# Performance work log

Hardware: AMD Instinct MI355X
Metric: run time of the kernel (lower is better)

The kernel has to match this reference:

```python
import jax, jax.numpy as jnp
import numpy as np

IMG = 224
PS = 2
C_IN = 3
EMBED = 768
BATCH = 256
SLICES = IMG // 2            # 112
L = 2 * (SLICES // PS)       # 112 levels
K = IMG * PS                 # 448 gathered (a,b) pairs per level
D_IN = K * C_IN              # 1344


def _build_levels(n=IMG, slices=SLICES, ps=PS):
    """Replicates LUnraveling index construction (natural order; set() in the
    original only permutes within a level, which is equivalent up to a fixed
    permutation of weight columns for random init)."""
    a_list, b_list = [], []
    ar = np.arange(n)
    for i in range(slices // ps):
        cols = range(i * ps, (i + 1) * ps)
        # 'up' level: pairs (j, col) for j in range(n), concatenated over ps cols
        a_list.append(np.concatenate([ar for _ in cols]))
        b_list.append(np.concatenate([np.full(n, c) for c in cols]))
        # 'right' level: pairs (n - slices + col, j) for j in range(n)
        a_list.append(np.concatenate([np.full(n, n - slices + c) for c in cols]))
        b_list.append(np.concatenate([ar for _ in cols]))
    return (np.stack(a_list).astype(np.int32), np.stack(b_list).astype(np.int32))


def setup_inputs() -> dict:
    key = jax.random.key(0)
    k1, k2, k3 = jax.random.split(key, 3)
    x = jax.random.normal(k1, (BATCH, C_IN, IMG, IMG), dtype=jnp.float32)
    W = jax.random.normal(k2, (EMBED, D_IN), dtype=jnp.float32) * (1.0 / np.sqrt(D_IN))
    b = jax.random.normal(k3, (EMBED,), dtype=jnp.float32) * 0.01
    a_np, b_np = _build_levels()
    return {"x": x, "W": W, "b": b,
            "a_idx": jnp.asarray(a_np), "b_idx": jnp.asarray(b_np)}


def reference(x, W, b, a_idx, b_idx):
    B = x.shape[0]
    # gather: x[:, :, a, b] with (L,K) index arrays -> (B, C, L, K)
    g = x[:, :, a_idx, b_idx]
    # per-level flatten(1) in torch flattens (C, K) C-major -> (B, L, C*K)
    g = jnp.transpose(g, (0, 2, 1, 3)).reshape(B, L, C_IN * K)
    # shared linear projection per level token
    tokens = jnp.einsum('bld,ed->ble', g, W) + b
    return tokens  # (B, L, EMBED); norm is Identity (norm_layer=None)
```

## Files before the change

kernel.cpp:

```cpp
#include <hip/hip_runtime.h>
#include <stdint.h>


#define IMG   224
#define NLEV  112
#define CIN   3
#define DIN   1344
#define EMB   768
#define BATCH 256
#define MTOT  28672
#define NT    21

#define BM    128
#define BN    128
#define BK    64
#define LDP   72

#define AS1 __attribute__((address_space(1)))
#define AS3 __attribute__((address_space(3)))

typedef __attribute__((ext_vector_type(8))) short   short8;
typedef __attribute__((ext_vector_type(4))) float   floatx4;

__device__ __forceinline__ unsigned short f2bf(float f) {
    unsigned u = __float_as_uint(f);
    unsigned r = (u + 0x7fffu + ((u >> 16) & 1u)) >> 16;
    return (unsigned short)r;
}
__device__ __forceinline__ float bf2f(unsigned short s) {
    return __uint_as_float(((unsigned)s) << 16);
}
__device__ __forceinline__ unsigned pack2(float a, float b) {
    return (unsigned)f2bf(a) | ((unsigned)f2bf(b) << 16);
}

__global__ void detect_dtype(const unsigned short* __restrict__ W, int* flag) {
    __shared__ int s;
    if (threadIdx.x == 0) s = 0;
    __syncthreads();
    int bad = 0;
    for (int k = threadIdx.x; k < 4096; k += 256) {
        unsigned v = (unsigned)W[2 * k] & 0x7FFFu;
        if (v >= 0x4000u) bad = 1;
    }
    if (bad) atomicOr(&s, 1);
    __syncthreads();
    if (threadIdx.x == 0) *flag = s;
}

__global__ __launch_bounds__(256)
void pack_w(const void* __restrict__ Wv, const void* __restrict__ Bv,
            unsigned short* __restrict__ Wb, float* __restrict__ Bf,
            const int* __restrict__ flag)
{
    const bool F32 = (*flag != 0);
    const int idx = blockIdx.x * 256 + threadIdx.x;
    if (F32) {
        const float4* s = (const float4*)((const float*)Wv + (size_t)idx * 8);
        float4 x0 = s[0], x1 = s[1];
        uint4 o;
        o.x = pack2(x0.x, x0.y); o.y = pack2(x0.z, x0.w);
        o.z = pack2(x1.x, x1.y); o.w = pack2(x1.z, x1.w);
        ((uint4*)Wb)[idx] = o;
    } else {
        ((uint4*)Wb)[idx] = ((const uint4*)Wv)[idx];
    }
    if (idx < EMB)
        Bf[idx] = F32 ? ((const float*)Bv)[idx]
                      : bf2f(((const unsigned short*)Bv)[idx]);
}

__global__ __launch_bounds__(256)
void pack_g(const void* __restrict__ Xv, unsigned short* __restrict__ Gc,
            int b0, const int* __restrict__ flag)
{
    const bool F32 = (*flag != 0);
    __shared__ __align__(16) unsigned short lds[IMG * 128];

    const int tid = threadIdx.x;
    const int bl  = blockIdx.x;
    const int c   = blockIdx.y;
    const size_t plane = ((size_t)(b0 + bl) * CIN + c) * (size_t)(IMG * IMG);
    unsigned short* Grow = Gc + (size_t)bl * NLEV * DIN + (size_t)c * 448;

    if (F32) {
        const float* src = (const float*)Xv + plane + (size_t)NLEV * IMG;
        for (int v = tid; v < 3136; v += 256) {
            const int i  = v / 56;
            const int kk = (v - i * 56) * 8;
            const float4* s = (const float4*)(src + (size_t)v * 8);
            float4 x0 = s[0], x1 = s[1];
            uint4 o;
            o.x = pack2(x0.x, x0.y); o.y = pack2(x0.z, x0.w);
            o.z = pack2(x1.x, x1.y); o.w = pack2(x1.z, x1.w);
            *(uint4*)(Grow + (size_t)(2 * i + 1) * DIN + kk) = o;
        }
    } else {
        const unsigned short* src = (const unsigned short*)Xv + plane + (size_t)NLEV * IMG;
        for (int v = tid; v < 3136; v += 256) {
            const int i  = v / 56;
            const int kk = (v - i * 56) * 8;
            *(uint4*)(Grow + (size_t)(2 * i + 1) * DIN + kk) =
                *(const uint4*)(src + (size_t)v * 8);
        }
    }

    for (int v = tid; v < 3136; v += 256) {
        const int r  = v / 14;
        const int vv = v - r * 14;
        const int key = (r >> 3) & 15;
        uint2 o0, o1;
        if (F32) {
            const float4* s = (const float4*)((const float*)Xv + plane
                              + (size_t)r * IMG + (size_t)vv * 8);
            float4 x0 = s[0], x1 = s[1];
            o0.x = pack2(x0.x, x0.y); o0.y = pack2(x0.z, x0.w);
            o1.x = pack2(x1.x, x1.y); o1.y = pack2(x1.z, x1.w);
        } else {
            const uint2* s = (const uint2*)((const unsigned short*)Xv + plane
                              + (size_t)r * IMG + (size_t)vv * 8);
            o0 = s[0]; o1 = s[1];
        }
        *(uint2*)&lds[r * 128 + ((2 * vv)     ^ key) * 4] = o0;
        *(uint2*)&lds[r * 128 + ((2 * vv + 1) ^ key) * 4] = o1;
    }
    __syncthreads();

    for (int idx = tid; idx < 56 * 56; idx += 256) {
        const int pr   = idx / 56;
        const int j    = idx - pr * 56;
        const int half = j / 28;
        const int r0   = (j - half * 28) * 8;
        const int qb   = pr >> 1;
        const int sh   = (pr & 1) * 2;
        unsigned short h[8];
        #pragma unroll
        for (int m = 0; m < 8; m++) {
            const int r = r0 + m;
            const unsigned v = *(const unsigned*)
                &lds[r * 128 + (qb ^ ((r >> 3) & 15)) * 4 + sh];
            h[m] = half ? (unsigned short)(v >> 16) : (unsigned short)(v & 0xFFFFu);
        }
        uint4 o;
        o.x = (unsigned)h[0] | ((unsigned)h[1] << 16);
        o.y = (unsigned)h[2] | ((unsigned)h[3] << 16);
        o.z = (unsigned)h[4] | ((unsigned)h[5] << 16);
        o.w = (unsigned)h[6] | ((unsigned)h[7] << 16);
        *(uint4*)(Grow + (size_t)(2 * pr) * DIN + half * IMG + r0) = o;
    }
}

__global__ __launch_bounds__(256)
void gemm_packed(const unsigned short* __restrict__ G,
                 const unsigned short* __restrict__ Wb,
                 const float* __restrict__ Bf,
                 float* __restrict__ Out)
{
    __shared__ __align__(16) unsigned short As[2][128 * 64];
    __shared__ __align__(16) unsigned short Bs[2][128 * 64];

    const int tid  = threadIdx.x;
    const int wave = tid >> 6;
    const int lane = tid & 63;

    const int bid = blockIdx.x;
    const int nwg = gridDim.x;
    const int q = nwg >> 3, r = nwg & 7;
    const int xcd = bid & 7, s = bid >> 3;
    const int lid = (xcd < r ? xcd * (q + 1) : r * (q + 1) + (xcd - r) * q) + s;
    const int mT = lid / 6;
    const int nT = lid - mT * 6;
    const int mBase = mT * 128;
    const int nBase = nT * 128;

    const int wm   = wave >> 1, wn = wave & 1;
    const int lrow = lane & 15;
    const int kq   = (lane >> 4) << 3;
    const int swz  = (lrow & 7) << 3;

    floatx4 acc[4][4];
    #pragma unroll
    for (int i = 0; i < 4; i++)
        #pragma unroll
        for (int j = 0; j < 4; j++)
            acc[i][j] = (floatx4){0.f, 0.f, 0.f, 0.f};

    const unsigned short* gaP[4];
    const unsigned short* gbP[4];
    unsigned ldsOff[4];
    #pragma unroll
    for (int i = 0; i < 4; i++) {
        const int idx = (i * 4 + wave) * 64 + lane;
        const int row = idx >> 3, k8 = idx & 7;
        const int jc  = k8 ^ (row & 7);
        gaP[i] = G  + (size_t)(mBase + row) * DIN + jc * 8;
        gbP[i] = Wb + (size_t)(nBase + row) * DIN + jc * 8;
        ldsOff[i] = (unsigned)((i * 4 + wave) * 512);
    }

    #pragma unroll
    for (int i = 0; i < 4; i++) {
        __builtin_amdgcn_global_load_lds((const AS1 void*)(gaP[i]),
                                         (AS3 void*)(&As[0][0] + ldsOff[i]), 16, 0, 0);
        __builtin_amdgcn_global_load_lds((const AS1 void*)(gbP[i]),
                                         (AS3 void*)(&Bs[0][0] + ldsOff[i]), 16, 0, 0);
    }
    __syncthreads();

    int cur = 0;
    for (int t = 0; t < NT; ++t) {
        if (t < NT - 1) {
            const int kt = (t + 1) * 64;
            #pragma unroll
            for (int i = 0; i < 4; i++) {
                __builtin_amdgcn_global_load_lds(
                    (const AS1 void*)(gaP[i] + kt),
                    (AS3 void*)(&As[cur ^ 1][0] + ldsOff[i]), 16, 0, 0);
                __builtin_amdgcn_global_load_lds(
                    (const AS1 void*)(gbP[i] + kt),
                    (AS3 void*)(&Bs[cur ^ 1][0] + ldsOff[i]), 16, 0, 0);
            }
        }
        const unsigned short* Ab = &As[cur][0];
        const unsigned short* Bb = &Bs[cur][0];
        #pragma unroll
        for (int k0 = 0; k0 < 64; k0 += 32) {
            short8 af[4], bfv[4];
            #pragma unroll
            for (int mi = 0; mi < 4; mi++)
                af[mi] = *(const short8*)&Ab[(wm * 64 + mi * 16 + lrow) * 64
                                             + ((k0 + kq) ^ swz)];
            #pragma unroll
            for (int ni = 0; ni < 4; ni++)
                bfv[ni] = *(const short8*)&Bb[(wn * 64 + ni * 16 + lrow) * 64
                                              + ((k0 + kq) ^ swz)];
            __builtin_amdgcn_s_setprio(1);
            #pragma unroll
            for (int mi = 0; mi < 4; mi++)
                #pragma unroll
                for (int ni = 0; ni < 4; ni++)
                    acc[mi][ni] = __builtin_amdgcn_mfma_f32_16x16x32_bf16(
                        af[mi], bfv[ni], acc[mi][ni], 0, 0, 0);
            __builtin_amdgcn_s_setprio(0);
        }
        __syncthreads();
        cur ^= 1;
    }

    const int quad = lane >> 4;
    #pragma unroll
    for (int ni = 0; ni < 4; ni++) {
        const int col = nBase + wn * 64 + ni * 16 + lrow;
        const float bv = Bf[col];
        #pragma unroll
        for (int mi = 0; mi < 4; mi++) {
            const int rbase = mBase + wm * 64 + mi * 16 + quad * 4;
            floatx4 a = acc[mi][ni];
            Out[(size_t)(rbase + 0) * EMB + col] = a[0] + bv;
            Out[(size_t)(rbase + 1) * EMB + col] = a[1] + bv;
            Out[(size_t)(rbase + 2) * EMB + col] = a[2] + bv;
            Out[(size_t)(rbase + 3) * EMB + col] = a[3] + bv;
        }
    }
}

template<bool F32>
__global__ __launch_bounds__(256, 2)
void lfreq_fused_gemm(const void* __restrict__ Xv,
                      const void* __restrict__ Wv,
                      const void* __restrict__ Bv,
                      const int* __restrict__ Aidx,
                      const int* __restrict__ Bidx,
                      float* __restrict__ Out,
                      const int* __restrict__ flag)
{
    if (*flag != (F32 ? 1 : 0)) return;

    __shared__ __align__(16) unsigned short As[BM][LDP];
    __shared__ __align__(16) unsigned short Bs[BN][LDP];

    const int tid   = threadIdx.x;
    const int wave  = tid >> 6;
    const int lane  = tid & 63;
    const int mBase = blockIdx.x * BM;
    const int nBase = blockIdx.y * BN;

    const int srow  = tid >> 1;
    const int shalf = tid & 1;
    const int am = mBase + srow;
    const int bb = am / NLEV;
    const int ll = am - bb * NLEV;

    floatx4 acc[4][4];
    #pragma unroll
    for (int i = 0; i < 4; i++)
        #pragma unroll
        for (int jj = 0; jj < 4; jj++)
            acc[i][jj] = (floatx4){0.f, 0.f, 0.f, 0.f};

    const int wm   = wave >> 1;
    const int wn   = wave & 1;
    const int lrow = lane & 15;
    const int kq   = (lane >> 4) << 3;

    for (int kt = 0; kt < DIN; kt += BK) {
        {
            const int koff = kt + shalf * 32;
            uint4* dst = (uint4*)&Bs[srow][shalf * 32];
            if (F32) {
                const float4* g = (const float4*)((const float*)Wv
                                + (size_t)(nBase + srow) * DIN + koff);
                #pragma unroll
                for (int q = 0; q < 4; q++) {
                    float4 v0 = g[2*q], v1 = g[2*q+1];
                    uint4 o;
                    o.x = pack2(v0.x, v0.y); o.y = pack2(v0.z, v0.w);
                    o.z = pack2(v1.x, v1.y); o.w = pack2(v1.z, v1.w);
                    dst[q] = o;
                }
            } else {
                const uint4* g = (const uint4*)((const unsigned short*)Wv
                               + (size_t)(nBase + srow) * DIN + koff);
                #pragma unroll
                for (int q = 0; q < 4; q++) dst[q] = g[q];
            }
        }
        {
            const int d0  = kt + shalf * 32;
            const int c   = (d0 >= 896) ? 2 : (d0 >= 448 ? 1 : 0);
            const int kk0 = d0 - c * 448;
            const int4* ap = (const int4*)(Aidx + ll * 448 + kk0);
            const int4* bp = (const int4*)(Bidx + ll * 448 + kk0);
            unsigned* du = (unsigned*)&As[srow][shalf * 32];
            if (F32) {
                const float* plane = (const float*)Xv
                    + (size_t)bb * (CIN * IMG * IMG) + (size_t)c * (IMG * IMG);
                #pragma unroll
                for (int q = 0; q < 8; q++) {
                    int4 av = ap[q], bv = bp[q];
                    du[2*q+0] = pack2(plane[av.x * IMG + bv.x], plane[av.y * IMG + bv.y]);
                    du[2*q+1] = pack2(plane[av.z * IMG + bv.z], plane[av.w * IMG + bv.w]);
                }
            } else {
                const unsigned short* plane = (const unsigned short*)Xv
                    + (size_t)bb * (CIN * IMG * IMG) + (size_t)c * (IMG * IMG);
                #pragma unroll
                for (int q = 0; q < 8; q++) {
                    int4 av = ap[q], bv = bp[q];
                    unsigned e0 = plane[av.x * IMG + bv.x];
                    unsigned e1 = plane[av.y * IMG + bv.y];
                    unsigned e2 = plane[av.z * IMG + bv.z];
                    unsigned e3 = plane[av.w * IMG + bv.w];
                    du[2*q+0] = e0 | (e1 << 16);
                    du[2*q+1] = e2 | (e3 << 16);
                }
            }
        }
        __syncthreads();

        #pragma unroll
        for (int k0 = 0; k0 < BK; k0 += 32) {
            short8 af[4], bfv[4];
            #pragma unroll
            for (int mi = 0; mi < 4; mi++)
                af[mi] = *(const short8*)&As[wm*64 + mi*16 + lrow][k0 + kq];
            #pragma unroll
            for (int ni = 0; ni < 4; ni++)
                bfv[ni] = *(const short8*)&Bs[wn*64 + ni*16 + lrow][k0 + kq];
            #pragma unroll
            for (int mi = 0; mi < 4; mi++)
                #pragma unroll
                for (int ni = 0; ni < 4; ni++)
                    acc[mi][ni] = __builtin_amdgcn_mfma_f32_16x16x32_bf16(
                        af[mi], bfv[ni], acc[mi][ni], 0, 0, 0);
        }
        __syncthreads();
    }

    const int quad = lane >> 4;
    #pragma unroll
    for (int ni = 0; ni < 4; ni++) {
        const int col = nBase + wn*64 + ni*16 + lrow;
        const float bv = F32 ? ((const float*)Bv)[col]
                             : bf2f(((const unsigned short*)Bv)[col]);
        #pragma unroll
        for (int mi = 0; mi < 4; mi++) {
            const int rbase = mBase + wm*64 + mi*16 + quad*4;
            floatx4 a = acc[mi][ni];
            Out[(size_t)(rbase+0)*EMB + col] = a[0] + bv;
            Out[(size_t)(rbase+1)*EMB + col] = a[1] + bv;
            Out[(size_t)(rbase+2)*EMB + col] = a[2] + bv;
            Out[(size_t)(rbase+3)*EMB + col] = a[3] + bv;
        }
    }
}

extern "C" void kernel_launch(void* const* d_in, const int* in_sizes, int n_in,
                              void* d_out, int out_size, void* d_ws, size_t ws_size,
                              hipStream_t stream) {
    const void* X    = d_in[0];
    const void* Wt   = d_in[1];
    const void* Bias = d_in[2];
    const int*  Ai   = (const int*)d_in[3];
    const int*  Bi   = (const int*)d_in[4];
    float* Out = (float*)d_out;

    char* ws  = (char*)d_ws;
    int* flag = (int*)ws;

    detect_dtype<<<dim3(1), dim3(256), 0, stream>>>((const unsigned short*)Wt, flag);

    float* Bf          = (float*)(ws + 256);
    unsigned short* Wb = (unsigned short*)(ws + 4096);
    const size_t gOff  = 4096 + (size_t)EMB * DIN * 2;
    unsigned short* Gc = (unsigned short*)(ws + gOff);

    int CHB = 0;
    const int cand[6] = {256, 128, 64, 32, 16, 8};
    for (int t = 0; t < 6; t++) {
        if (gOff + (size_t)cand[t] * NLEV * DIN * 2 <= ws_size) { CHB = cand[t]; break; }
    }

    if (CHB == 0) {
        dim3 grid(MTOT / BM, EMB / BN);
        lfreq_fused_gemm<false><<<grid, dim3(256), 0, stream>>>(X, Wt, Bias, Ai, Bi, Out, flag);
        lfreq_fused_gemm<true ><<<grid, dim3(256), 0, stream>>>(X, Wt, Bias, Ai, Bi, Out, flag);
        return;
    }

    pack_w<<<dim3(504), dim3(256), 0, stream>>>(Wt, Bias, Wb, Bf, flag);

    for (int b0 = 0; b0 < BATCH; b0 += CHB) {
        dim3 pgrid(CHB, CIN);
        pack_g<<<pgrid, dim3(256), 0, stream>>>(X, Gc, b0, flag);
        dim3 ggrid(CHB * NLEV / 128 * 6);
        gemm_packed<<<ggrid, dim3(256), 0, stream>>>(Gc, Wb, Bf,
                                                     Out + (size_t)b0 * NLEV * EMB);
    }
}
```

Measured before the change: 346.4 us.

## Fuse dtype detection and weight packing into gather kernel, relax GEMM barriers

Merges the separate dtype-detect, weight-pack and gather-pack kernels into one launch: each block re-checks the weight dtype with a smaller sample in shared memory, and an extra grid row packs W and bias. This removes two kernel launches and the dependency on a global flag. The GEMM main loop replaces __syncthreads with explicit vmcnt waits plus raw barriers, so the prefetch of the next tile can stay in flight while the current tile is consumed. It risks subtle LDS races if the vmcnt count is wrong, and the reduced dtype sample is less robust.

New measurement: 334.0 us. 1.04x faster.

```diff
diff --git a/kernel.cpp b/kernel.cpp
--- a/kernel.cpp
+++ b/kernel.cpp
@@ -49,37 +49,56 @@
 }
 
 __global__ __launch_bounds__(256)
-void pack_w(const void* __restrict__ Wv, const void* __restrict__ Bv,
-            unsigned short* __restrict__ Wb, float* __restrict__ Bf,
-            const int* __restrict__ flag)
+void pack_all(const void* __restrict__ Xv, const void* __restrict__ Wv,
+              const void* __restrict__ Bv,
+              unsigned short* __restrict__ Gc, unsigned short* __restrict__ Wb,
+              float* __restrict__ Bf, int b0, int chb, int doW)
 {
-    const bool F32 = (*flag != 0);
-    const int idx = blockIdx.x * 256 + threadIdx.x;
-    if (F32) {
-        const float4* s = (const float4*)((const float*)Wv + (size_t)idx * 8);
-        float4 x0 = s[0], x1 = s[1];
-        uint4 o;
-        o.x = pack2(x0.x, x0.y); o.y = pack2(x0.z, x0.w);
-        o.z = pack2(x1.x, x1.y); o.w = pack2(x1.z, x1.w);
-        ((uint4*)Wb)[idx] = o;
-    } else {
-        ((uint4*)Wb)[idx] = ((const uint4*)Wv)[idx];
-    }
-    if (idx < EMB)
-        Bf[idx] = F32 ? ((const float*)Bv)[idx]
-                      : bf2f(((const unsigned short*)Bv)[idx]);
-}
-
-__global__ __launch_bounds__(256)
-void pack_g(const void* __restrict__ Xv, unsigned short* __restrict__ Gc,
-            int b0, const int* __restrict__ flag)
-{
-    const bool F32 = (*flag != 0);
     __shared__ __align__(16) unsigned short lds[IMG * 128];
+    __shared__ int sflag;
 
     const int tid = threadIdx.x;
-    const int bl  = blockIdx.x;
-    const int c   = blockIdx.y;
+
+    {
+        if (tid == 0) sflag = 0;
+        int bad = 0;
+        const unsigned short* Wu = (const unsigned short*)Wv;
+        #pragma unroll
+        for (int k = tid; k < 512; k += 256) {
+            unsigned v = (unsigned)Wu[2 * k] & 0x7FFFu;
+            if (v >= 0x4000u) bad = 1;
+        }
+        __syncthreads();
+        if (bad) atomicOr(&sflag, 1);
+        __syncthreads();
+    }
+    const bool F32 = (sflag != 0);
+
+    if (blockIdx.y == 3) {
+        if (!doW) return;
+        const int total = EMB * DIN / 8;
+        for (int idx = blockIdx.x * 256 + tid; idx < total; idx += chb * 256) {
+            if (F32) {
+                const float4* s = (const float4*)((const float*)Wv + (size_t)idx * 8);
+                float4 x0 = s[0], x1 = s[1];
+                uint4 o;
+                o.x = pack2(x0.x, x0.y); o.y = pack2(x0.z, x0.w);
+                o.z = pack2(x1.x, x1.y); o.w = pack2(x1.z, x1.w);
+                ((uint4*)Wb)[idx] = o;
+            } else {
+                ((uint4*)Wb)[idx] = ((const uint4*)Wv)[idx];
+            }
+        }
+        if (blockIdx.x == 0) {
+            for (int e = tid; e < EMB; e += 256)
+                Bf[e] = F32 ? ((const float*)Bv)[e]
+                            : bf2f(((const unsigned short*)Bv)[e]);
+        }
+        return;
+    }
+
+    const int bl = blockIdx.x;
+    const int c  = blockIdx.y;
     const size_t plane = ((size_t)(b0 + bl) * CIN + c) * (size_t)(IMG * IMG);
     unsigned short* Grow = Gc + (size_t)bl * NLEV * DIN + (size_t)c * 448;
 
@@ -205,7 +224,6 @@
         __builtin_amdgcn_global_load_lds((const AS1 void*)(gbP[i]),
                                          (AS3 void*)(&Bs[0][0] + ldsOff[i]), 16, 0, 0);
     }
-    __syncthreads();
 
     int cur = 0;
     for (int t = 0; t < NT; ++t) {
@@ -220,7 +238,13 @@
                     (const AS1 void*)(gbP[i] + kt),
                     (AS3 void*)(&Bs[cur ^ 1][0] + ldsOff[i]), 16, 0, 0);
             }
-        }
+            asm volatile("s_waitcnt vmcnt(8)" ::: "memory");
+        } else {
+            asm volatile("s_waitcnt vmcnt(0)" ::: "memory");
+        }
+        __builtin_amdgcn_s_barrier();
+        __builtin_amdgcn_sched_barrier(0);
+
         const unsigned short* Ab = &As[cur][0];
         const unsigned short* Bb = &Bs[cur][0];
         #pragma unroll
@@ -243,7 +267,8 @@
                         af[mi], bfv[ni], acc[mi][ni], 0, 0, 0);
             __builtin_amdgcn_s_setprio(0);
         }
-        __syncthreads();
+        __builtin_amdgcn_s_barrier();
+        __builtin_amdgcn_sched_barrier(0);
         cur ^= 1;
     }
 
@@ -408,8 +433,6 @@
     char* ws  = (char*)d_ws;
     int* flag = (int*)ws;
 
-    detect_dtype<<<dim3(1), dim3(256), 0, stream>>>((const unsigned short*)Wt, flag);
-
     float* Bf          = (float*)(ws + 256);
     unsigned short* Wb = (unsigned short*)(ws + 4096);
     const size_t gOff  = 4096 + (size_t)EMB * DIN * 2;
@@ -422,17 +445,17 @@
     }
 
     if (CHB == 0) {
+        detect_dtype<<<dim3(1), dim3(256), 0, stream>>>((const unsigned short*)Wt, flag);
         dim3 grid(MTOT / BM, EMB / BN);
         lfreq_fused_gemm<false><<<grid, dim3(256), 0, stream>>>(X, Wt, Bias, Ai, Bi, Out, flag);
         lfreq_fused_gemm<true ><<<grid, dim3(256), 0, stream>>>(X, Wt, Bias, Ai, Bi, Out, flag);
         return;
     }
 
-    pack_w<<<dim3(504), dim3(256), 0, stream>>>(Wt, Bias, Wb, Bf, flag);
-
     for (int b0 = 0; b0 < BATCH; b0 += CHB) {
-        dim3 pgrid(CHB, CIN);
-        pack_g<<<pgrid, dim3(256), 0, stream>>>(X, Gc, b0, flag);
+        dim3 pgrid(CHB, 4);
+        pack_all<<<pgrid, dim3(256), 0, stream>>>(X, Wt, Bias, Gc, Wb, Bf,
+                                                  b0, CHB, b0 == 0 ? 1 : 0);
         dim3 ggrid(CHB * NLEV / 128 * 6);
         gemm_packed<<<ggrid, dim3(256), 0, stream>>>(Gc, Wb, Bf,
                                                      Out + (size_t)b0 * NLEV * EMB);
```
